# Optimization experiments

Hardware: AMD Instinct MI355X
Metric: run time of the kernel (lower is better)

The kernel has to match this reference:

```python
import jax, jax.numpy as jnp
import numpy as np
from jax import lax

B, H, W, C = 2, 256, 256, 192
HEADS = 6
WS = 8                      # window size
PW = WS // 2                # permuted window size (kv downsampled 2x2)
HIDDEN = 4 * C
HEAD_DIM = C // HEADS
SCALE = HEAD_DIM ** -0.5
N_WIN = WS * WS             # 64 query tokens per window
N_KV = PW * PW              # 16 kv tokens per window


def _aligned_index(pw0, pw1):
    ch = np.arange(pw0)
    cw = np.arange(pw1)
    coords = np.stack(np.meshgrid(ch, cw, indexing='ij'))          # (2, pw0, pw1)
    cf = coords.reshape(2, -1)
    rel = (cf[:, :, None] - cf[:, None, :]).transpose(1, 2, 0).astype(np.int64)
    rel[:, :, 0] += pw0 - 1
    rel[:, :, 1] += pw1 - 1
    rel[:, :, 0] *= 2 * pw1 - 1
    idx = rel.sum(-1)                                              # (N_KV, N_KV)
    n4 = pw0 * pw1
    idx = idx.reshape(pw0, pw1, 1, 1, n4)
    idx = np.tile(idx, (1, 1, 2, 2, 1)).transpose(0, 2, 1, 3, 4).reshape(4 * n4, n4)
    return jnp.asarray(idx)

IDX = _aligned_index(PW, PW)   # (N_WIN, N_KV)


def layernorm(x, g, b):
    mu = x.mean(-1, keepdims=True)
    var = ((x - mu) ** 2).mean(-1, keepdims=True)
    return (x - mu) * lax.rsqrt(var + 1e-5) * g + b


def window_partition(x):
    # (B, H, W, C) -> (B*nW, WS, WS, C)
    x = x.reshape(B, H // WS, WS, W // WS, WS, C)
    return x.transpose(0, 1, 3, 2, 4, 5).reshape(-1, WS, WS, C)


def window_reverse(w):
    # (B*nW, WS, WS, C) -> (B, H, W, C)
    x = w.reshape(B, H // WS, W // WS, WS, WS, C)
    return x.transpose(0, 1, 3, 2, 4, 5).reshape(B, H, W, C)


def setup_inputs() -> dict:
    key = jax.random.key(0)
    ks = jax.random.split(key, 10)
    rn = lambda k, shp, s=0.02: jax.random.normal(k, shp, jnp.float32) * s
    return {
        'x': jax.random.normal(ks[0], (B, H * W, C), jnp.float32),
        'g1': jnp.ones((C,), jnp.float32), 'be1': jnp.zeros((C,), jnp.float32),
        'wq': rn(ks[1], (C, C)), 'bq': jnp.zeros((C,), jnp.float32),
        'wkv': rn(ks[2], (C, C // 2)), 'bkv': jnp.zeros((C // 2,), jnp.float32),
        'bias_table': rn(ks[3], ((2 * PW - 1) * (2 * PW - 1), HEADS)),
        'wproj': rn(ks[4], (C, C)), 'bproj': jnp.zeros((C,), jnp.float32),
        'g2': jnp.ones((C,), jnp.float32), 'be2': jnp.zeros((C,), jnp.float32),
        'w1f': rn(ks[5], (C, HIDDEN)), 'b1f': jnp.zeros((HIDDEN,), jnp.float32),
        'dwk': rn(ks[6], (HIDDEN, 1, 5, 5)), 'dwb': jnp.zeros((HIDDEN,), jnp.float32),
        'w2f': rn(ks[7], (HIDDEN, C)), 'b2f': jnp.zeros((C,), jnp.float32),
    }


def reference(x, g1, be1, wq, bq, wkv, bkv, bias_table, wproj, bproj,
              g2, be2, w1f, b1f, dwk, dwb, w2f, b2f):
    shortcut = x
    xn = layernorm(x, g1, be1).reshape(B, H, W, C)
    xw = window_partition(xn).reshape(-1, N_WIN, C)        # (b_, 64, C)
    b_ = xw.shape[0]
    # PSA: kv downsampled 2x2 spatially, 2x2 block folded into channels
    kv = (xw @ wkv + bkv).reshape(b_, PW, 2, PW, 2, 2, C // 4)
    kv = kv.transpose(0, 1, 3, 5, 2, 4, 6).reshape(b_, N_KV, 2, HEADS, HEAD_DIM)
    kv = kv.transpose(2, 0, 3, 1, 4)                       # (2, b_, h, N_KV, d)
    k, v = kv[0], kv[1]
    q = (xw @ wq + bq).reshape(b_, N_WIN, HEADS, HEAD_DIM).transpose(0, 2, 1, 3) * SCALE
    attn = jnp.einsum('bhqd,bhkd->bhqk', q, k)             # (b_, h, 64, 16)
    bias = bias_table[IDX.reshape(-1)].reshape(N_WIN, N_KV, HEADS).transpose(2, 0, 1)
    attn = jax.nn.softmax(attn + bias[None], axis=-1)
    aw = jnp.einsum('bhqk,bhkd->bhqd', attn, v).transpose(0, 2, 1, 3).reshape(b_, N_WIN, C)
    aw = aw @ wproj + bproj
    x = shortcut + window_reverse(aw.reshape(-1, WS, WS, C)).reshape(B, H * W, C)
    # ConvFFN with depthwise-conv residual branch
    xn2 = layernorm(x, g2, be2)
    h1 = jax.nn.gelu(xn2 @ w1f + b1f, approximate=False)   # (B, HW, HIDDEN)
    img = h1.transpose(0, 2, 1).reshape(B, HIDDEN, H, W)
    conv = lax.conv_general_dilated(img, dwk, (1, 1), ((2, 2), (2, 2)),
                                    feature_group_count=HIDDEN,
                                    dimension_numbers=('NCHW', 'OIHW', 'NCHW'))
    conv = jax.nn.gelu(conv + dwb[None, :, None, None], approximate=False)
    h = h1 + conv.reshape(B, HIDDEN, H * W).transpose(0, 2, 1)
    return x + (h @ w2f + b2f)
```

## Files before the change

### kernel.cpp

```cpp
#include <hip/hip_runtime.h>
#include <hip/hip_bf16.h>
#include <math.h>

#define NTOK  131072
#define NTOKH 65536
#define CD    192
#define HID   768


typedef short bf16x8 __attribute__((ext_vector_type(8)));
typedef float f32x4  __attribute__((ext_vector_type(4)));
typedef float f32x2  __attribute__((ext_vector_type(2)));
typedef __bf16 bf16x2_t __attribute__((ext_vector_type(2)));

__device__ __forceinline__ float bf2f(unsigned short v) {
    union { unsigned int u; float f; } c; c.u = ((unsigned int)v) << 16; return c.f;
}
__device__ __forceinline__ unsigned short f2bf(float f) {
    union { float f; unsigned int u; } c; c.f = f;
    unsigned int r = c.u + 0x7FFFu + ((c.u >> 16) & 1u);
    return (unsigned short)(r >> 16);
}
__device__ __forceinline__ float lo_bf(unsigned p) {
    union { unsigned u; float f; } c; c.u = p << 16; return c.f;
}
__device__ __forceinline__ float hi_bf(unsigned p) {
    union { unsigned u; float f; } c; c.u = p & 0xFFFF0000u; return c.f;
}
__device__ __forceinline__ float dot2bf(unsigned a, unsigned b, float c) {
#if __has_builtin(__builtin_amdgcn_fdot2_f32_bf16)
    union U { unsigned u; bf16x2_t v; };
    U ua, ub; ua.u = a; ub.u = b;
    return __builtin_amdgcn_fdot2_f32_bf16(ua.v, ub.v, c, false);
#else
    return fmaf(hi_bf(a) , hi_bf(b), fmaf(lo_bf(a), lo_bf(b), c));
#endif
}
__device__ __forceinline__ float gelu_f(float x) {
    float t = x * 0.7071067811865476f;
    t = fminf(fmaxf(t, -4.0f), 4.0f);
    float s2 = t * t;
    float p = fmaf(s2, -2.72614225801306e-10f, 2.77068142495902e-08f);
    p = fmaf(s2, p, -2.10102402082508e-06f);
    p = fmaf(s2, p, -5.69250639462346e-05f);
    p = fmaf(s2, p, -7.34990630326855e-04f);
    p = fmaf(s2, p, -2.95459980854025e-03f);
    p = fmaf(s2, p, -1.60960333262415e-02f);
    p = p * t;
    float q = fmaf(s2, -1.45660718464996e-05f, -2.13374055278905e-04f);
    q = fmaf(s2, q, -1.68282697438203e-03f);
    q = fmaf(s2, q, -7.37332916720468e-03f);
    q = fmaf(s2, q, -1.42647390514189e-02f);
    float er = p * __builtin_amdgcn_rcpf(q);
    return 0.5f * x * (1.0f + er);
}

__device__ __forceinline__ void gld16(const unsigned short* g, unsigned short* l) {
    __builtin_amdgcn_global_load_lds(
        (const __attribute__((address_space(1))) void*)(unsigned long long)(g),
        (__attribute__((address_space(3))) void*)(unsigned int)(unsigned long long)(l),
        16, 0, 0);
}

__global__ __launch_bounds__(256) void ln_kernel(const float* __restrict__ x,
                                                 const float* __restrict__ g,
                                                 const float* __restrict__ b,
                                                 unsigned short* __restrict__ out) {
    int tok  = blockIdx.x * 4 + (threadIdx.x >> 6);
    int lane = threadIdx.x & 63;
    const float* xp = x + (size_t)tok * CD;
    float v0 = xp[lane], v1 = xp[lane + 64], v2 = xp[lane + 128];
    float s  = v0 + v1 + v2;
    float s2 = v0 * v0 + v1 * v1 + v2 * v2;
    #pragma unroll
    for (int off = 32; off > 0; off >>= 1) {
        s  += __shfl_xor(s,  off, 64);
        s2 += __shfl_xor(s2, off, 64);
    }
    float mu  = s * (1.0f / 192.0f);
    float var = s2 * (1.0f / 192.0f) - mu * mu;
    float rs  = rsqrtf(var + 1e-5f);
    unsigned short* op = out + (size_t)tok * CD;
    op[lane]       = f2bf((v0 - mu) * rs * g[lane]       + b[lane]);
    op[lane + 64]  = f2bf((v1 - mu) * rs * g[lane + 64]  + b[lane + 64]);
    op[lane + 128] = f2bf((v2 - mu) * rs * g[lane + 128] + b[lane + 128]);
}

__global__ __launch_bounds__(256) void wconv_kernel(
    const float* __restrict__ wq, const float* __restrict__ wkv,
    const float* __restrict__ wproj, const float* __restrict__ w1f,
    const float* __restrict__ w2f,
    unsigned short* __restrict__ qkvT, unsigned short* __restrict__ projT,
    unsigned short* __restrict__ w1T, unsigned short* __restrict__ w2T)
{
    int i = blockIdx.x * 256 + threadIdx.x;
    if (i < 288 * 192) {
        int n = i / 192, k = i - n * 192;
        float v = (n < 192) ? wq[(size_t)k * 192 + n] : wkv[(size_t)k * 96 + (n - 192)];
        qkvT[n * 192 + k] = f2bf(v);
    }
    if (i < 192 * 192) {
        int n = i / 192, k = i - n * 192;
        projT[n * 192 + k] = f2bf(wproj[(size_t)k * 192 + n]);
    }
    {
        int n = i / 192, k = i - n * 192;
        w1T[n * 192 + k] = f2bf(w1f[(size_t)k * 768 + n]);
    }
    {
        int n = i / 768, k = i - n * 768;
        w2T[n * 768 + k] = f2bf(w2f[(size_t)k * 192 + n]);
    }
}

__global__ __launch_bounds__(256) void dwprep_kernel(
    const float* __restrict__ dwk, unsigned int* __restrict__ pP, float* __restrict__ pS)
{
    int i = blockIdx.x * 256 + threadIdx.x;
    if (i >= 768 * 5) return;
    const float* w = dwk + (size_t)i * 5;
    unsigned b0 = f2bf(w[0]), b1 = f2bf(w[1]), b2 = f2bf(w[2]),
             b3 = f2bf(w[3]), b4 = f2bf(w[4]);
    pP[i * 4 + 0] = b0 | (b1 << 16);
    pP[i * 4 + 1] = b2 | (b3 << 16);
    pP[i * 4 + 2] = b1 | (b2 << 16);
    pP[i * 4 + 3] = b3 | (b4 << 16);
    pS[i * 2 + 0] = w[0];
    pS[i * 2 + 1] = w[4];
}

__device__ __forceinline__ void xcd_swz(int gx, int& bx, int& by) {
    int nwg  = gx * (int)gridDim.y;
    int id   = (int)blockIdx.y * gx + (int)blockIdx.x;
    int q    = nwg >> 3, r = nwg & 7;
    int xcd  = id & 7, rest = id >> 3;
    int sw   = (xcd < r ? xcd * (q + 1) : r * (q + 1) + (xcd - r) * q) + rest;
    bx = sw % gx; by = sw / gx;
}

template<int MODE>
__global__ __launch_bounds__(256) void mgemm_kernel(
    const unsigned short* __restrict__ A,
    const unsigned short* __restrict__ WT,
    const float* __restrict__ b0, const float* __restrict__ b1,
    const float* __restrict__ addsrc,
    void* O0, unsigned short* __restrict__ O1,
    int K, int Nreal)
{
    constexpr int BM = 128, BN = 96, BK = 32;
    __shared__ unsigned short As[2][BM * BK];
    __shared__ unsigned short Bs[2][BN * BK];
    const int tid  = threadIdx.x;
    const int wave = tid >> 6, lane = tid & 63;
    const int quad = lane >> 4, l16 = lane & 15;
    const int wm = (wave >> 1) * 64, wn = (wave & 1) * 48;
    int bx, by; xcd_swz(gridDim.x, bx, by);
    const int m0 = by * BM, n0 = bx * BN;

    f32x4 acc[4][3];
    #pragma unroll
    for (int mi = 0; mi < 4; mi++)
        #pragma unroll
        for (int ni = 0; ni < 3; ni++) acc[mi][ni] = (f32x4){0.f, 0.f, 0.f, 0.f};

    const int r16 = lane >> 2;
    const int sw  = ((lane & 3) ^ ((r16 >> 1) & 3)) << 3;
    const unsigned short* aS0 = A + (size_t)(m0 + wave * 32      + r16) * K + sw;
    const unsigned short* aS1 = A + (size_t)(m0 + wave * 32 + 16 + r16) * K + sw;
    const int bc0 = (wave < 2) ? wave * 2     : 4 + (wave - 2);
    const int bc1 = (wave < 2) ? wave * 2 + 1 : -1;
    const unsigned short* bS0 = WT + (size_t)(n0 + bc0 * 16 + r16) * K + sw;
    const unsigned short* bS1 = WT + (size_t)(n0 + (bc1 < 0 ? 0 : bc1) * 16 + r16) * K + sw;
    unsigned short* aD0 = &As[0][(wave * 32) * BK];
    unsigned short* aD1 = &As[0][(wave * 32 + 16) * BK];
    unsigned short* bD0 = &Bs[0][(bc0 * 16) * BK];
    unsigned short* bD1 = &Bs[0][((bc1 < 0 ? 0 : bc1) * 16) * BK];
    const int bufStrA = BM * BK;
    const int bufStrB = BN * BK;

    const int nt = K / BK;
    {
        gld16(aS0, aD0); gld16(aS1, aD1); gld16(bS0, bD0);
        if (bc1 >= 0) gld16(bS1, bD1);
    }
    __syncthreads();

    int cur = 0;
    for (int t = 0; t < nt; ++t) {
        if (t + 1 < nt) {
            int ko = (t + 1) * BK;
            int nb = (cur ^ 1);
            gld16(aS0 + ko, aD0 + nb * bufStrA);
            gld16(aS1 + ko, aD1 + nb * bufStrA);
            gld16(bS0 + ko, bD0 + nb * bufStrB);
            if (bc1 >= 0) gld16(bS1 + ko, bD1 + nb * bufStrB);
        }
        bf16x8 bfr[3];
        #pragma unroll
        for (int ni = 0; ni < 3; ni++) {
            int br = wn + ni * 16 + l16;
            bfr[ni] = *(const bf16x8*)&Bs[cur][br * BK + ((quad ^ ((br >> 1) & 3)) << 3)];
        }
        #pragma unroll
        for (int mi = 0; mi < 4; mi++) {
            int ar = wm + mi * 16 + l16;
            bf16x8 af = *(const bf16x8*)&As[cur][ar * BK + ((quad ^ ((ar >> 1) & 3)) << 3)];
            acc[mi][0] = __builtin_amdgcn_mfma_f32_16x16x32_bf16(af, bfr[0], acc[mi][0], 0, 0, 0);
            acc[mi][1] = __builtin_amdgcn_mfma_f32_16x16x32_bf16(af, bfr[1], acc[mi][1], 0, 0, 0);
            acc[mi][2] = __builtin_amdgcn_mfma_f32_16x16x32_bf16(af, bfr[2], acc[mi][2], 0, 0, 0);
        }
        __syncthreads();
        cur ^= 1;
    }

    float bc[3], bcc1[3];
    #pragma unroll
    for (int ni = 0; ni < 3; ni++) {
        int col = n0 + wn + ni * 16 + l16;
        if (MODE == 0) {
            if (n0 < 192) bc[ni] = b0[col];
            else          bcc1[ni] = b1[col - 192];
        } else {
            bc[ni] = b0[col];
        }
    }
    #pragma unroll
    for (int mi = 0; mi < 4; mi++) {
        int row0 = m0 + wm + mi * 16 + quad * 4;
        #pragma unroll
        for (int r = 0; r < 4; r++) {
            unsigned mrow = (unsigned)(row0 + r);
            if (MODE == 0) {
                if (n0 < 192) {
                    unsigned ob = mrow * 192u + (unsigned)(n0 + wn + l16);
                    unsigned short* q0 = (unsigned short*)O0;
                    #pragma unroll
                    for (int ni = 0; ni < 3; ni++)
                        q0[ob + ni * 16] = f2bf((acc[mi][ni][r] + bc[ni]) * 0.17677669529663687f);
                } else {
                    unsigned ob = mrow * 96u + (unsigned)(n0 - 192 + wn + l16);
                    #pragma unroll
                    for (int ni = 0; ni < 3; ni++)
                        O1[ob + ni * 16] = f2bf(acc[mi][ni][r] + bcc1[ni]);
                }
            } else if (MODE == 1) {
                unsigned ob = mrow * 192u + (unsigned)(n0 + wn + l16);
                float* op = (float*)O0;
                #pragma unroll
                for (int ni = 0; ni < 3; ni++)
                    op[ob + ni * 16] = acc[mi][ni][r] + bc[ni] + addsrc[ob + ni * 16];
            } else if (MODE == 2) {
                unsigned ob = mrow * 768u + (unsigned)(n0 + wn + l16);
                unsigned short* op = (unsigned short*)O0;
                #pragma unroll
                for (int ni = 0; ni < 3; ni++)
                    op[ob + ni * 16] = f2bf(gelu_f(acc[mi][ni][r] + bc[ni]));
            } else {
                unsigned ob = mrow * 192u + (unsigned)(n0 + wn + l16);
                float* op = (float*)O0;
                #pragma unroll
                for (int ni = 0; ni < 3; ni++)
                    op[ob + ni * 16] = op[ob + ni * 16] + acc[mi][ni][r] + bc[ni];
            }
        }
    }
}

__global__ __launch_bounds__(384) void attn_kernel(
    const unsigned short* __restrict__ q, const unsigned short* __restrict__ kvp,
    const float* __restrict__ bt, unsigned short* __restrict__ aw)
{
    __shared__ float ks[6][16][32];
    __shared__ float vs[6][16][32];
    const int w = blockIdx.x;
    const int b = w >> 10, rem = w & 1023, wh = rem >> 5, wc = rem & 31;
    const int tid = threadIdx.x;
    const size_t base = (size_t)b * 65536;

    for (int e = tid; e < 16 * 192; e += 384) {
        int kk = e / 192, f = e - kk * 192;
        int d1 = kk >> 2, d3 = kk & 3;
        int d2 = f / 96;  int r = f - d2 * 96;
        int d4 = r / 48;  int c4 = r - d4 * 48;
        int i = 2 * d1 + d2, j = 2 * d3 + d4;
        size_t g = base + (size_t)(wh * 8 + i) * 256 + (wc * 8 + j);
        int h = f >> 5, d = f & 31;
        ks[h][kk][d] = bf2f(kvp[g * 96 + c4]);
        vs[h][kk][d] = bf2f(kvp[g * 96 + 48 + c4]);
    }
    __syncthreads();

    const int t = tid & 63, h = tid >> 6;
    const int i = t >> 3, j = t & 7;
    const int iq2 = i >> 1, jq2 = j >> 1;
    const size_t g = base + (size_t)(wh * 8 + i) * 256 + (wc * 8 + j);

    f32x2 qr[16];
    const ushort4* qp = (const ushort4*)(q + g * 192 + h * 32);
    #pragma unroll
    for (int d4i = 0; d4i < 8; d4i++) {
        ushort4 u = qp[d4i];
        qr[d4i * 2 + 0] = (f32x2){bf2f(u.x), bf2f(u.y)};
        qr[d4i * 2 + 1] = (f32x2){bf2f(u.z), bf2f(u.w)};
    }

    float lg[16]; float mx = -1e30f;
    #pragma unroll
    for (int kk = 0; kk < 16; kk++) {
        int kh = kk >> 2, kw = kk & 3;
        const f32x2* kp = (const f32x2*)&ks[h][kk][0];
        f32x2 a2 = (f32x2){bt[((iq2 - kh + 3) * 7 + (jq2 - kw + 3)) * 6 + h], 0.f};
        #pragma unroll
        for (int d = 0; d < 16; d++) a2 = __builtin_elementwise_fma(qr[d], kp[d], a2);
        float s = a2.x + a2.y;
        lg[kk] = s; mx = fmaxf(mx, s);
    }
    float den = 0.f;
    #pragma unroll
    for (int kk = 0; kk < 16; kk++) { lg[kk] = expf(lg[kk] - mx); den += lg[kk]; }
    float inv = 1.0f / den;

    f32x2 oacc[16];
    #pragma unroll
    for (int d = 0; d < 16; d++) oacc[d] = (f32x2){0.f, 0.f};
    #pragma unroll
    for (int kk = 0; kk < 16; kk++) {
        float p = lg[kk] * inv;
        f32x2 pv = (f32x2){p, p};
        const f32x2* vp = (const f32x2*)&vs[h][kk][0];
        #pragma unroll
        for (int d = 0; d < 16; d++) oacc[d] = __builtin_elementwise_fma(pv, vp[d], oacc[d]);
    }
    unsigned int* op = (unsigned int*)(aw + g * 192 + h * 32);
    #pragma unroll
    for (int d = 0; d < 16; d++) {
        unsigned int lo = f2bf(oacc[d].x), hi = f2bf(oacc[d].y);
        op[d] = lo | (hi << 16);
    }
}

__global__ __launch_bounds__(256) void dwconv_kernel(
    const unsigned short* __restrict__ h1,
    const float* __restrict__ dwk, const float* __restrict__ dwb,
    const unsigned int* __restrict__ pP, const float* __restrict__ pS,
    unsigned short* __restrict__ hout)
{
    __shared__ unsigned short tile[12][12][64];
    int bx = blockIdx.x;
    int chb = bx % 12; int t = bx / 12;
    int tw = t % 32; int th = t / 32;
    const int tid = threadIdx.x;
    const int chbase = chb * 64;
    const int ch = tid & 63;
    const int cp = tid >> 6;
    const int c0 = cp * 2;
    const int gch = chbase + ch;
    const float bias = dwb[gch];

    const int lane4 = tid & 15;
    const int pg = tid >> 4;

#if __has_builtin(__builtin_amdgcn_fdot2_f32_bf16)
    unsigned wA[5][2], wB[5][2]; float w0s[5], w4s[5];
    #pragma unroll
    for (int kr = 0; kr < 5; kr++) {
        int idx = gch * 5 + kr;
        wA[kr][0] = pP[idx * 4 + 0];
        wA[kr][1] = pP[idx * 4 + 1];
        wB[kr][0] = pP[idx * 4 + 2];
        wB[kr][1] = pP[idx * 4 + 3];
        w0s[kr]   = pS[idx * 2 + 0];
        w4s[kr]   = pS[idx * 2 + 1];
    }
    for (int p = pg; p < 144; p += 16) {
        int pr = p / 12, pc = p - pr * 12;
        int r = th * 8 - 2 + pr, c = tw * 8 - 2 + pc;
        ushort4 u = make_ushort4(0, 0, 0, 0);
        if (r >= 0 && r < 256 && c >= 0 && c < 256)
            u = *(const ushort4*)(h1 + (((size_t)r * 256 + c) * HID + chbase + lane4 * 4));
        *(ushort4*)&tile[pr][pc][lane4 * 4] = u;
    }
    __syncthreads();

    unsigned pw[5][3];
    #pragma unroll
    for (int rr = 0; rr < 4; rr++)
        #pragma unroll
        for (int j = 0; j < 3; j++)
            pw[rr][j] = (unsigned)tile[rr][c0 + 2 * j][ch]
                      | ((unsigned)tile[rr][c0 + 2 * j + 1][ch] << 16);

    unsigned obase = ((unsigned)(th * 8) * 256u + (unsigned)(tw * 8 + c0)) * (unsigned)HID
                   + (unsigned)gch;

    #pragma unroll
    for (int r0 = 0; r0 < 8; r0++) {
        const int rn = (r0 + 4) % 5;
        #pragma unroll
        for (int j = 0; j < 3; j++)
            pw[rn][j] = (unsigned)tile[r0 + 4][c0 + 2 * j][ch]
                      | ((unsigned)tile[r0 + 4][c0 + 2 * j + 1][ch] << 16);

        float s0 = bias, s1 = bias;
        #pragma unroll
        for (int kr = 0; kr < 5; kr++) {
            const int ri = (r0 + kr) % 5;
            s0 = dot2bf(pw[ri][0], wA[kr][0], s0);
            s0 = dot2bf(pw[ri][1], wA[kr][1], s0);
            s0 = fmaf(lo_bf(pw[ri][2]), w4s[kr], s0);
            s1 = fmaf(hi_bf(pw[ri][0]), w0s[kr], s1);
            s1 = dot2bf(pw[ri][1], wB[kr][0], s1);
            s1 = dot2bf(pw[ri][2], wB[kr][1], s1);
        }
        const int rc = (r0 + 2) % 5;
        float v0 = lo_bf(pw[rc][1]) + gelu_f(s0);
        float v1 = hi_bf(pw[rc][1]) + gelu_f(s1);
        hout[obase]       = f2bf(v0);
        hout[obase + HID] = f2bf(v1);
        obase += 256u * (unsigned)HID;
    }
#else
    float w[25];
    #pragma unroll
    for (int tap = 0; tap < 25; tap++)
        w[tap] = dwk[(size_t)gch * 25 + tap];
    for (int p = pg; p < 144; p += 16) {
        int pr = p / 12, pc = p - pr * 12;
        int r = th * 8 - 2 + pr, c = tw * 8 - 2 + pc;
        ushort4 u = make_ushort4(0, 0, 0, 0);
        if (r >= 0 && r < 256 && c >= 0 && c < 256)
            u = *(const ushort4*)(h1 + (((size_t)r * 256 + c) * HID + chbase + lane4 * 4));
        *(ushort4*)&tile[pr][pc][lane4 * 4] = u;
    }
    __syncthreads();
    float win[5][6];
    #pragma unroll
    for (int rr = 0; rr < 4; rr++)
        #pragma unroll
        for (int cc = 0; cc < 6; cc++)
            win[rr][cc] = bf2f(tile[rr][c0 + cc][ch]);
    unsigned obase = ((unsigned)(th * 8) * 256u + (unsigned)(tw * 8 + c0)) * (unsigned)HID
                   + (unsigned)gch;
    #pragma unroll
    for (int r0 = 0; r0 < 8; r0++) {
        #pragma unroll
        for (int cc = 0; cc < 6; cc++)
            win[(r0 + 4) % 5][cc] = bf2f(tile[r0 + 4][c0 + cc][ch]);
        float s0 = bias, s1 = bias;
        #pragma unroll
        for (int kr = 0; kr < 5; kr++) {
            int ri = (r0 + kr) % 5;
            #pragma unroll
            for (int kc = 0; kc < 5; kc++) {
                float wt = w[kr * 5 + kc];
                s0 = fmaf(win[ri][kc],     wt, s0);
                s1 = fmaf(win[ri][kc + 1], wt, s1);
            }
        }
        const int rc = (r0 + 2) % 5;
        float v0 = win[rc][2] + gelu_f(s0);
        float v1 = win[rc][3] + gelu_f(s1);
        hout[obase]       = f2bf(v0);
        hout[obase + HID] = f2bf(v1);
        obase += 256u * (unsigned)HID;
    }
#endif
}

extern "C" void kernel_launch(void* const* d_in, const int* in_sizes, int n_in,
                              void* d_out, int out_size, void* d_ws, size_t ws_size,
                              hipStream_t stream) {
    const float* x    = (const float*)d_in[0];
    const float* g1   = (const float*)d_in[1];
    const float* be1  = (const float*)d_in[2];
    const float* wq   = (const float*)d_in[3];
    const float* bq   = (const float*)d_in[4];
    const float* wkv  = (const float*)d_in[5];
    const float* bkv  = (const float*)d_in[6];
    const float* btab = (const float*)d_in[7];
    const float* wproj= (const float*)d_in[8];
    const float* bproj= (const float*)d_in[9];
    const float* g2   = (const float*)d_in[10];
    const float* be2  = (const float*)d_in[11];
    const float* w1f  = (const float*)d_in[12];
    const float* b1f  = (const float*)d_in[13];
    const float* dwk  = (const float*)d_in[14];
    const float* dwb  = (const float*)d_in[15];
    const float* w2f  = (const float*)d_in[16];
    const float* b2f  = (const float*)d_in[17];
    float* out = (float*)d_out;

    char* ws = (char*)d_ws;
    unsigned short* xnb  = (unsigned short*)(ws);
    unsigned short* qb   = (unsigned short*)(ws + 50331648);
    unsigned short* kvb  = (unsigned short*)(ws + 100663296);
    unsigned short* h1b  = (unsigned short*)(ws + 125829120);
    unsigned short* hhb  = (unsigned short*)(ws + 226492416);
    unsigned short* qkvT = (unsigned short*)(ws + 327155712);
    unsigned short* projT= (unsigned short*)(ws + 327266304);
    unsigned short* w1T  = (unsigned short*)(ws + 327340032);
    unsigned short* w2T  = (unsigned short*)(ws + 327634944);
    unsigned int* dwpP = (unsigned int*)(ws);
    float*        dwpS = (float*)(ws + 61440);

    wconv_kernel<<<576, 256, 0, stream>>>(wq, wkv, wproj, w1f, w2f,
                                          qkvT, projT, w1T, w2T);
    ln_kernel<<<NTOK / 4, 256, 0, stream>>>(x, g1, be1, xnb);
    mgemm_kernel<0><<<dim3(3, NTOK / 128), 256, 0, stream>>>(
        xnb, qkvT, bq, bkv, nullptr, qb, kvb, 192, 288);
    attn_kernel<<<2048, 384, 0, stream>>>(qb, kvb, btab, xnb);
    mgemm_kernel<1><<<dim3(2, NTOK / 128), 256, 0, stream>>>(
        xnb, projT, bproj, nullptr, x, out, nullptr, 192, 192);
    dwprep_kernel<<<15, 256, 0, stream>>>(dwk, dwpP, dwpS);
    ln_kernel<<<NTOK / 4, 256, 0, stream>>>(out, g2, be2, qb);
    for (int half = 0; half < 2; half++) {
        const unsigned short* xn2h = qb + (size_t)half * NTOKH * CD;
        float* outh = out + (size_t)half * NTOKH * CD;
        mgemm_kernel<2><<<dim3(8, NTOKH / 128), 256, 0, stream>>>(
            xn2h, w1T, b1f, nullptr, nullptr, h1b, nullptr, 192, 768);
        dwconv_kernel<<<12 * 32 * 32, 256, 0, stream>>>(h1b, dwk, dwb, dwpP, dwpS, hhb);
        mgemm_kernel<3><<<dim3(2, NTOKH / 128), 256, 0, stream>>>(
            hhb, w2T, b2f, nullptr, nullptr, outh, nullptr, 768, 192);
    }
}
```

Before: 752.5 us.

## Fuse projection GEMM, residual add, and second LayerNorm into one kernel

Replaces the proj GEMM (MODE 1) and the separate LN2 kernel with one kernel. Each block owns a full 128x192 row tile, so the per-row mean and variance can be reduced in registers and shared memory and written directly as bf16 xn2. This removes one kernel launch and one fp32 read of the full activation tensor. The cost is fewer blocks (1024 of 512 threads), a single-pass variance formula, and extra shared-memory reduction work in the epilogue.

```diff
diff --git a/kernel.cpp b/kernel.cpp
--- a/kernel.cpp
+++ b/kernel.cpp
@@ -243,12 +243,6 @@
                     for (int ni = 0; ni < 3; ni++)
                         O1[ob + ni * 16] = f2bf(acc[mi][ni][r] + bcc1[ni]);
                 }
-            } else if (MODE == 1) {
-                unsigned ob = mrow * 192u + (unsigned)(n0 + wn + l16);
-                float* op = (float*)O0;
-                #pragma unroll
-                for (int ni = 0; ni < 3; ni++)
-                    op[ob + ni * 16] = acc[mi][ni][r] + bc[ni] + addsrc[ob + ni * 16];
             } else if (MODE == 2) {
                 unsigned ob = mrow * 768u + (unsigned)(n0 + wn + l16);
                 unsigned short* op = (unsigned short*)O0;
@@ -262,6 +256,132 @@
                 for (int ni = 0; ni < 3; ni++)
                     op[ob + ni * 16] = op[ob + ni * 16] + acc[mi][ni][r] + bc[ni];
             }
+        }
+    }
+}
+
+__global__ __launch_bounds__(512) void projln_kernel(
+    const unsigned short* __restrict__ A,
+    const unsigned short* __restrict__ WT,
+    const float* __restrict__ bpj,
+    const float* __restrict__ xres,
+    const float* __restrict__ g2, const float* __restrict__ be2,
+    float* __restrict__ out, unsigned short* __restrict__ xn2)
+{
+    constexpr int BM = 128, BN = 192, BK = 32, K = 192;
+    __shared__ unsigned short As[2][BM * BK];
+    __shared__ unsigned short Bs[2][BN * BK];
+    const int tid  = threadIdx.x;
+    const int wave = tid >> 6, lane = tid & 63;
+    const int quad = lane >> 4, l16 = lane & 15;
+    const int wr = wave >> 2, wc = wave & 3;
+    const int wm = wr * 64, wn = wc * 48;
+    int id = blockIdx.x;
+    int swzb = (id & 7) * 128 + (id >> 3);
+    const int m0 = swzb * BM;
+
+    f32x4 acc[4][3];
+    #pragma unroll
+    for (int mi = 0; mi < 4; mi++)
+        #pragma unroll
+        for (int ni = 0; ni < 3; ni++) acc[mi][ni] = (f32x4){0.f, 0.f, 0.f, 0.f};
+
+    const int r16 = lane >> 2;
+    const int sw  = ((lane & 3) ^ ((r16 >> 1) & 3)) << 3;
+    const unsigned short* aS0 = A + (size_t)(m0 + wave * 16 + r16) * K + sw;
+    const int brow0 = (wave < 4) ? wave * 32 : 128 + 16 * (wave - 4);
+    const bool hasB1 = (wave < 4);
+    const unsigned short* bS0 = WT + (size_t)(brow0 + r16) * K + sw;
+    const unsigned short* bS1 = WT + (size_t)(brow0 + 16 + r16) * K + sw;
+    unsigned short* aD0 = &As[0][(wave * 16) * BK];
+    unsigned short* bD0 = &Bs[0][brow0 * BK];
+    unsigned short* bD1 = &Bs[0][(brow0 + 16) * BK];
+    const int bufStrA = BM * BK;
+    const int bufStrB = BN * BK;
+
+    const int nt = K / BK;
+    {
+        gld16(aS0, aD0); gld16(bS0, bD0);
+        if (hasB1) gld16(bS1, bD1);
+    }
+    __syncthreads();
+
+    int cur = 0;
+    for (int t = 0; t < nt; ++t) {
+        if (t + 1 < nt) {
+            int ko = (t + 1) * BK;
+            int nb = (cur ^ 1);
+            gld16(aS0 + ko, aD0 + nb * bufStrA);
+            gld16(bS0 + ko, bD0 + nb * bufStrB);
+            if (hasB1) gld16(bS1 + ko, bD1 + nb * bufStrB);
+        }
+        bf16x8 bfr[3];
+        #pragma unroll
+        for (int ni = 0; ni < 3; ni++) {
+            int br = wn + ni * 16 + l16;
+            bfr[ni] = *(const bf16x8*)&Bs[cur][br * BK + ((quad ^ ((br >> 1) & 3)) << 3)];
+        }
+        #pragma unroll
+        for (int mi = 0; mi < 4; mi++) {
+            int ar = wm + mi * 16 + l16;
+            bf16x8 af = *(const bf16x8*)&As[cur][ar * BK + ((quad ^ ((ar >> 1) & 3)) << 3)];
+            acc[mi][0] = __builtin_amdgcn_mfma_f32_16x16x32_bf16(af, bfr[0], acc[mi][0], 0, 0, 0);
+            acc[mi][1] = __builtin_amdgcn_mfma_f32_16x16x32_bf16(af, bfr[1], acc[mi][1], 0, 0, 0);
+            acc[mi][2] = __builtin_amdgcn_mfma_f32_16x16x32_bf16(af, bfr[2], acc[mi][2], 0, 0, 0);
+        }
+        __syncthreads();
+        cur ^= 1;
+    }
+
+    float bcp[3], g2c[3], be2c[3];
+    #pragma unroll
+    for (int ni = 0; ni < 3; ni++) {
+        int col = wn + ni * 16 + l16;
+        bcp[ni] = bpj[col]; g2c[ni] = g2[col]; be2c[ni] = be2[col];
+    }
+    float* red = (float*)&As[0][0];
+    #pragma unroll
+    for (int mi = 0; mi < 4; mi++) {
+        #pragma unroll
+        for (int r = 0; r < 4; r++) {
+            int row = wm + mi * 16 + quad * 4 + r;
+            unsigned ob = (unsigned)(m0 + row) * 192u + (unsigned)(wn + l16);
+            float ps = 0.f, ps2 = 0.f;
+            #pragma unroll
+            for (int ni = 0; ni < 3; ni++) {
+                float y = acc[mi][ni][r] + bcp[ni] + xres[ob + ni * 16];
+                out[ob + ni * 16] = y;
+                acc[mi][ni][r] = y;
+                ps += y; ps2 += y * y;
+            }
+            #pragma unroll
+            for (int off = 1; off < 16; off <<= 1) {
+                ps  += __shfl_xor(ps,  off, 64);
+                ps2 += __shfl_xor(ps2, off, 64);
+            }
+            if (l16 == 0) {
+                red[(row * 4 + wc) * 2 + 0] = ps;
+                red[(row * 4 + wc) * 2 + 1] = ps2;
+            }
+        }
+    }
+    __syncthreads();
+    #pragma unroll
+    for (int mi = 0; mi < 4; mi++) {
+        #pragma unroll
+        for (int r = 0; r < 4; r++) {
+            int row = wm + mi * 16 + quad * 4 + r;
+            float S1 = red[(row * 4 + 0) * 2 + 0] + red[(row * 4 + 1) * 2 + 0]
+                     + red[(row * 4 + 2) * 2 + 0] + red[(row * 4 + 3) * 2 + 0];
+            float S2 = red[(row * 4 + 0) * 2 + 1] + red[(row * 4 + 1) * 2 + 1]
+                     + red[(row * 4 + 2) * 2 + 1] + red[(row * 4 + 3) * 2 + 1];
+            float mu  = S1 * (1.0f / 192.0f);
+            float var = S2 * (1.0f / 192.0f) - mu * mu;
+            float rs  = rsqrtf(var + 1e-5f);
+            unsigned ob = (unsigned)(m0 + row) * 192u + (unsigned)(wn + l16);
+            #pragma unroll
+            for (int ni = 0; ni < 3; ni++)
+                xn2[ob + ni * 16] = f2bf((acc[mi][ni][r] - mu) * rs * g2c[ni] + be2c[ni]);
         }
     }
 }
@@ -509,10 +629,9 @@
     mgemm_kernel<0><<<dim3(3, NTOK / 128), 256, 0, stream>>>(
         xnb, qkvT, bq, bkv, nullptr, qb, kvb, 192, 288);
     attn_kernel<<<2048, 384, 0, stream>>>(qb, kvb, btab, xnb);
-    mgemm_kernel<1><<<dim3(2, NTOK / 128), 256, 0, stream>>>(
-        xnb, projT, bproj, nullptr, x, out, nullptr, 192, 192);
+    projln_kernel<<<1024, 512, 0, stream>>>(
+        xnb, projT, bproj, x, g2, be2, out, qb);
     dwprep_kernel<<<15, 256, 0, stream>>>(dwk, dwpP, dwpS);
-    ln_kernel<<<NTOK / 4, 256, 0, stream>>>(out, g2, be2, qb);
     for (int half = 0; half < 2; half++) {
         const unsigned short* xn2h = qb + (size_t)half * NTOKH * CD;
         float* outh = out + (size_t)half * NTOKH * CD;
```

New measurement: 757.6 us. No clear change (+0.7%).
